# Optimization experiments

Measured on AMD Instinct MI355X. Metric: run time of the kernel, lower is better.

## Reference

```python
import jax, jax.numpy as jnp
import numpy as np

LEAKY_SLOPE = 0.01  # torch nn.LeakyReLU default

def leaky_relu(x):
    return jnp.where(x >= 0, x, LEAKY_SLOPE * x)

def setup_inputs() -> dict:
    key = jax.random.key(0)
    ks = jax.random.split(key, 11)
    B, F, C_IN, H, K, D = 2048, 512, 3, 64, 8, 128  # batch, features, expand, layer_conf[0], bucket_num, bucket_dim
    ASR, MM, OUT = 128, 768, 256
    proj_in = ASR + MM + F * D
    inp = {
        "stat_features": jax.random.uniform(ks[0], (B, F), dtype=jnp.float32),
        "asr_embeddings": jax.random.normal(ks[1], (B, ASR), dtype=jnp.float32),
        "mm_embeddings": jax.random.normal(ks[2], (B, MM), dtype=jnp.float32),
        "linear1_w": jax.random.normal(ks[3], (F, C_IN, H), dtype=jnp.float32) * (1.0 / np.sqrt(C_IN)),
        "linear1_b": jax.random.normal(ks[4], (F, 1, H), dtype=jnp.float32),
        "linear2_w": jax.random.normal(ks[5], (F, H, K), dtype=jnp.float32) * (1.0 / np.sqrt(H)),
        "linear2_b": jax.random.normal(ks[6], (F, 1, K), dtype=jnp.float32),
        "tau": jnp.ones((F, 1, K), dtype=jnp.float32),
        "emb": jax.random.normal(ks[7], (F, K, D), dtype=jnp.float32),
        "proj_w": jax.random.normal(ks[8], (OUT, proj_in), dtype=jnp.float32) * (1.0 / np.sqrt(proj_in)),
        "proj_b": jax.random.normal(ks[9], (OUT,), dtype=jnp.float32) * 0.01,
    }
    return inp

def reference(stat_features, asr_embeddings, mm_embeddings,
              linear1_w, linear1_b, linear2_w, linear2_b, tau, emb,
              proj_w, proj_b):
    # sanitize: NaN -> 0, negatives -> 0
    x = stat_features
    x = jnp.where(jnp.isnan(x) | (x < 0.0), 0.0, x)  # [B, F]

    # auto_dis: per-feature tiny MLP. x is expanded to 3 identical copies -> [B,F,1,3]
    # matmul with [F,3,H] == einsum over the 3 copies.
    B, F = x.shape
    x3 = jnp.broadcast_to(x[:, :, None], (B, F, 3))           # [B,F,3]
    h = jnp.einsum('bfc,fch->bfh', x3, linear1_w) + linear1_b[:, 0, :]  # [B,F,H]
    h = jnp.where(h >= 0, h, LEAKY_SLOPE * h)
    s = jnp.einsum('bfh,fhk->bfk', h, linear2_w) + linear2_b[:, 0, :]   # [B,F,K]
    s = jnp.where(s >= 0, s, LEAKY_SLOPE * s)
    s = s * tau[:, 0, :]
    p = jax.nn.softmax(s, axis=-1)                            # [B,F,K]
    y = jnp.einsum('bfk,fkd->bfd', p, emb)                    # [B,F,D]
    y = y.reshape(B, -1)                                      # [B, F*D] (fc = Identity)

    z = jnp.concatenate([asr_embeddings, mm_embeddings, y], axis=1)
    out = jax.nn.relu(z @ proj_w.T + proj_b)                  # [B, 256]
    return out
```

## Files before the change

kernel.cpp:

```cpp
#include <hip/hip_runtime.h>
#include <hip/hip_bf16.h>
#include <math.h>

#define LEAKY 0.01f
#define B_    2048
#define F_    512
#define H_    64
#define K_    8
#define D_    128
#define ASR_  128
#define MM_   768
#define OUT_  256
#define PROJ_IN 66432
#define ZK    4992
#define NSPLIT 8


typedef unsigned short u16;
typedef u16   u16x8 __attribute__((ext_vector_type(8)));
typedef short s16x8 __attribute__((ext_vector_type(8)));
typedef float f32x4 __attribute__((ext_vector_type(4)));

__device__ __forceinline__ u16 f2bf(float x) {
  unsigned int u = __float_as_uint(x);
  u += 0x7fffu + ((u >> 16) & 1u);
  return (u16)(u >> 16);
}

__device__ __forceinline__ float quad_sum(float g) {
  int a = __builtin_amdgcn_update_dpp(0, __float_as_int(g), 0xB1, 0xF, 0xF, true);
  g += __int_as_float(a);
  int b = __builtin_amdgcn_update_dpp(0, __float_as_int(g), 0x4E, 0xF, 0xF, true);
  return g + __int_as_float(b);
}

#define PRODUCER_BLOCKS (512 + 1024 + 896 + 224)

__global__ __launch_bounds__(256) void producer_kernel(
    const float* __restrict__ stat, const float* __restrict__ w1,
    const float* __restrict__ b1v, const float* __restrict__ w2,
    const float* __restrict__ b2v, const float* __restrict__ tauv,
    const float* __restrict__ pw, const float* __restrict__ emb,
    const float* __restrict__ asr, const float* __restrict__ mm,
    u16* __restrict__ A0, u16* __restrict__ Pf, u16* __restrict__ Wn) {
  __shared__ __align__(16) char smem[15616];
  const int bid = blockIdx.x;
  const int t = threadIdx.x;

  if (bid < 512) {
    const int f0 = (bid >> 3) * 8;
    const int o0 = (bid & 7) * 32;
    const int w = t >> 6, lam = t & 63;
    const int fl = lam >> 5, k = (lam >> 2) & 7, dq = lam & 3;
    const int fbase = f0 + 2 * w;
    float* sw = (float*)smem + w * 512;
    float* buf0 = sw;
    float* buf1 = sw + 256;
    const int wslot = lam ^ ((lam >> 3) & 7);
    const int xr = fl * 4 + dq;
    float4 e[8];
    {
      const float* ep = emb + ((size_t)(fbase + fl) * 8 + k) * 128 + dq * 32;
      #pragma unroll
      for (int j = 0; j < 8; ++j) e[j] = *(const float4*)(ep + j * 4);
    }
    const float* gsrc = pw + 896 + (size_t)fbase * 128
                        + (size_t)o0 * PROJ_IN + lam * 4;
    u16* wdst = Wn + (size_t)o0 * ZK + 896 + (size_t)(fbase + fl) * 8 + k;
    const float* rd0 = buf0 + fl * 128 + dq * 32;
    const float* rd1 = buf1 + fl * 128 + dq * 32;
#define LDR(R) (*(const float4*)(gsrc + (size_t)(R) * PROJ_IN))
#define WNG_ROW(BUF, RD, VREG, R, NEXT)                                       \
    {                                                                         \
      *(float4*)((BUF) + wslot * 4) = VREG;           \
      if ((NEXT) < 32) VREG = LDR(NEXT);                    \
      float g0 = 0.f, g1 = 0.f;                                               \
      _Pragma("unroll")                                                       \
      for (int j = 0; j < 8; ++j) {                                           \
        float4 p4 = *(const float4*)((RD) + 4 * (j ^ xr));                    \
        g0 = fmaf(e[j].x, p4.x, g0);                                          \
        g1 = fmaf(e[j].y, p4.y, g1);                                          \
        g0 = fmaf(e[j].z, p4.z, g0);                                          \
        g1 = fmaf(e[j].w, p4.w, g1);                                          \
      }                                                                       \
      float g = quad_sum(g0 + g1);                                            \
      if (dq == 0) wdst[(size_t)(R) * ZK] = f2bf(g);                          \
    }
    float4 va = LDR(0), vb = LDR(1), vc = LDR(2), vd = LDR(3);
    for (int gi = 0; gi < 8; ++gi) {
      const int r = 4 * gi;
      WNG_ROW(buf0, rd0, va, r,     r + 4);
      WNG_ROW(buf1, rd1, vb, r + 1, r + 5);
      WNG_ROW(buf0, rd0, vc, r + 2, r + 6);
      WNG_ROW(buf1, rd1, vd, r + 3, r + 7);
    }
#undef WNG_ROW
#undef LDR
  } else if (bid < 1536) {
    const int pb = bid - 512;
    const int f0 = (pb & 127) * 4;
    const int b0 = (pb >> 7) * 256;
    float* s_w1s = (float*)(smem);
    float* s_b1  = (float*)(smem + 1024);
    float* s_x   = (float*)(smem + 2048);
    {
      int fl = t >> 6, h = t & 63;
      const float* wf = w1 + (size_t)(f0 + fl) * 192;
      s_w1s[fl * 64 + h] = wf[h] + wf[64 + h] + wf[128 + h];
      s_b1[fl * 64 + h] = b1v[(size_t)(f0 + fl) * 64 + h];
    }
    {
      float4 sv = *(const float4*)(stat + (size_t)(b0 + t) * F_ + f0);
      float* xr_ = s_x + t * 5;
      xr_[0] = (sv.x >= 0.f) ? sv.x : 0.f;
      xr_[1] = (sv.y >= 0.f) ? sv.y : 0.f;
      xr_[2] = (sv.z >= 0.f) ? sv.z : 0.f;
      xr_[3] = (sv.w >= 0.f) ? sv.w : 0.f;
    }
    __syncthreads();

    const int w = t >> 6;
    const int wu = __builtin_amdgcn_readfirstlane(w);
    const int lane = t & 63;
    const float* w1p = s_w1s + w * 64;
    const float* b1p = s_b1 + w * 64;
    const float* w2u  = w2   + (size_t)(f0 + wu) * 512;
    const float* b2u  = b2v  + (size_t)(f0 + wu) * 8;
    const float* tauu = tauv + (size_t)(f0 + wu) * 8;
    float x[4];
    #pragma unroll
    for (int p = 0; p < 4; ++p) x[p] = s_x[(lane + 64 * p) * 5 + w];
    float acc[4][8] = {{0.f}};
    #pragma unroll 4
    for (int i = 0; i < 64; ++i) {
      float wv = w1p[i], bv = b1p[i];
      float4 wa = *(const float4*)(w2u + i * 8);
      float4 wb = *(const float4*)(w2u + i * 8 + 4);
      #pragma unroll
      for (int p = 0; p < 4; ++p) {
        float h0 = fmaf(x[p], wv, bv);
        float h = fmaf(LEAKY, fminf(h0, 0.f), fmaxf(h0, 0.f));
        acc[p][0] = fmaf(h, wa.x, acc[p][0]);
        acc[p][1] = fmaf(h, wa.y, acc[p][1]);
        acc[p][2] = fmaf(h, wa.z, acc[p][2]);
        acc[p][3] = fmaf(h, wa.w, acc[p][3]);
        acc[p][4] = fmaf(h, wb.x, acc[p][4]);
        acc[p][5] = fmaf(h, wb.y, acc[p][5]);
        acc[p][6] = fmaf(h, wb.z, acc[p][6]);
        acc[p][7] = fmaf(h, wb.w, acc[p][7]);
      }
    }
    #pragma unroll
    for (int p = 0; p < 4; ++p) {
      float s[K_];
      float m = -1e30f;
      #pragma unroll
      for (int kk = 0; kk < K_; ++kk) {
        float v = acc[p][kk] + b2u[kk];
        v = (v >= 0.f) ? v : LEAKY * v;
        v *= tauu[kk];
        s[kk] = v;
        m = fmaxf(m, v);
      }
      float sum = 0.f;
      #pragma unroll
      for (int kk = 0; kk < K_; ++kk) { s[kk] = __expf(s[kk] - m); sum += s[kk]; }
      float inv = 1.f / sum;
      u16x8 hv;
      #pragma unroll
      for (int kk = 0; kk < K_; ++kk) hv[kk] = f2bf(s[kk] * inv);
      *(u16x8*)(Pf + ((size_t)(f0 + w) * B_ + b0 + lane + 64 * p) * 8) = hv;
    }
  } else if (bid < 2432) {
    const int item = bid - 1536;
    const int cidx = item * 256 + t;
    const int r = cidx / 112, c = cidx % 112;
    float4 v0, v1;
    if (c < 16) {
      const float* s = asr + (size_t)r * ASR_ + c * 8;
      v0 = *(const float4*)(s); v1 = *(const float4*)(s + 4);
    } else {
      const float* s = mm + (size_t)r * MM_ + (c - 16) * 8;
      v0 = *(const float4*)(s); v1 = *(const float4*)(s + 4);
    }
    u16x8 hv = {f2bf(v0.x), f2bf(v0.y), f2bf(v0.z), f2bf(v0.w),
                f2bf(v1.x), f2bf(v1.y), f2bf(v1.z), f2bf(v1.w)};
    *(u16x8*)(A0 + (size_t)r * 896 + c * 8) = hv;
  } else {
    const int item = bid - 2432;
    #pragma unroll
    for (int rr = 0; rr < 4; ++rr) {
      int idx = item * 1024 + rr * 256 + t;
      int o = idx / 896, j = idx % 896;
      Wn[(size_t)o * ZK + j] = f2bf(pw[(size_t)o * PROJ_IN + j]);
    }
  }
}

#define SAS 72
__global__ __launch_bounds__(256) void gemm_kernel(
    const u16* __restrict__ A0, const u16* __restrict__ Pf,
    const u16* __restrict__ Wn, float* __restrict__ part) {
  const int bm0 = blockIdx.x * 64;
  const int bn0 = blockIdx.y * 64;
  const int kz  = blockIdx.z;
  const int it0 = kz * 10;
  const int itn = (kz == 7) ? 8 : 10;
  __shared__ u16 sA[64 * SAS];
  __shared__ u16 sB[64 * SAS];
  const int t = threadIdx.x;
  const int w = t >> 6, L = t & 63;
  const int l16 = L & 15, q8 = (L >> 4) * 8;
  const int wm = (w >> 1) * 32, wn = (w & 1) * 32;
  const int row = t >> 2, lk = t & 3;
  const int pp = t >> 5, pg = t & 31;
  f32x4 acc[2][2] = {{{0.f,0.f,0.f,0.f},{0.f,0.f,0.f,0.f}},
                     {{0.f,0.f,0.f,0.f},{0.f,0.f,0.f,0.f}}};
  u16x8 ra[2], rb[2];

#define LOAD_TILES(IT)                                                        \
  {                                                                           \
    const int k0_ = (IT) * 64;                                                \
    if (k0_ < 896) {                                                          \
      const u16* s_ = A0 + (size_t)(bm0 + row) * 896 + k0_ + lk * 8;          \
      ra[0] = *(const u16x8*)(s_);                                            \
      ra[1] = *(const u16x8*)(s_ + 32);                                       \
    } else {                                                                  \
      const int fb_ = (k0_ - 896) >> 3;                                       \
      const u16* s_ = Pf + ((size_t)(fb_ + pp) * B_ + bm0 + pg) * 8;          \
      ra[0] = *(const u16x8*)(s_);                                            \
      ra[1] = *(const u16x8*)(s_ + 256);                        \
    }                                                                         \
    const u16* sb_ = Wn + (size_t)(bn0 + row) * ZK + k0_ + lk * 8;            \
    rb[0] = *(const u16x8*)(sb_);                                             \
    rb[1] = *(const u16x8*)(sb_ + 32);                                        \
  }

#define STORE_TILES(IT)                                                       \
  {                                                                           \
    if ((IT) * 64 < 896) {                                                    \
      *(u16x8*)&sA[row * SAS + lk * 8]      = ra[0];                          \
      *(u16x8*)&sA[row * SAS + lk * 8 + 32] = ra[1];                          \
    } else {                                                                  \
      *(u16x8*)&sA[pg * SAS + pp * 8]        = ra[0];                         \
      *(u16x8*)&sA[(pg + 32) * SAS + pp * 8] = ra[1];                         \
    }                                                                         \
    *(u16x8*)&sB[row * SAS + lk * 8]      = rb[0];                            \
    *(u16x8*)&sB[row * SAS + lk * 8 + 32] = rb[1];                            \
  }

  LOAD_TILES(it0);
  for (int it = it0; it < it0 + itn; ++it) {
    __syncthreads();
    STORE_TILES(it);
    __syncthreads();
    if (it + 1 < it0 + itn) LOAD_TILES(it + 1);
    #pragma unroll
    for (int ks = 0; ks < 2; ++ks) {
      s16x8 a0 = *(const s16x8*)&sA[(wm + l16) * SAS + ks * 32 + q8];
      s16x8 a1 = *(const s16x8*)&sA[(wm + 16 + l16) * SAS + ks * 32 + q8];
      s16x8 b0 = *(const s16x8*)&sB[(wn + l16) * SAS + ks * 32 + q8];
      s16x8 b1 = *(const s16x8*)&sB[(wn + 16 + l16) * SAS + ks * 32 + q8];
      acc[0][0] = __builtin_amdgcn_mfma_f32_16x16x32_bf16(a0, b0, acc[0][0], 0, 0, 0);
      acc[0][1] = __builtin_amdgcn_mfma_f32_16x16x32_bf16(a0, b1, acc[0][1], 0, 0, 0);
      acc[1][0] = __builtin_amdgcn_mfma_f32_16x16x32_bf16(a1, b0, acc[1][0], 0, 0, 0);
      acc[1][1] = __builtin_amdgcn_mfma_f32_16x16x32_bf16(a1, b1, acc[1][1], 0, 0, 0);
    }
  }
#undef LOAD_TILES
#undef STORE_TILES

  float* dst = part + (size_t)kz * B_ * OUT_;
  #pragma unroll
  for (int mf = 0; mf < 2; ++mf) {
    const int r0 = bm0 + wm + mf * 16 + (L >> 4) * 4;
    #pragma unroll
    for (int nf = 0; nf < 2; ++nf) {
      const int col = bn0 + wn + nf * 16 + l16;
      #pragma unroll
      for (int i = 0; i < 4; ++i)
        dst[(size_t)(r0 + i) * OUT_ + col] = acc[mf][nf][i];
    }
  }
}

__global__ __launch_bounds__(256) void combine_kernel(
    const float* __restrict__ part, const float* __restrict__ pb,
    float* __restrict__ out) {
  const int idx4 = (blockIdx.x * 256 + threadIdx.x) * 4;
  const int o = idx4 & (OUT_ - 1);
  float4 bv = *(const float4*)(pb + o);
  float4 r = bv;
  #pragma unroll
  for (int kz = 0; kz < NSPLIT; ++kz) {
    float4 a = *(const float4*)(part + (size_t)kz * B_ * OUT_ + idx4);
    r.x += a.x; r.y += a.y; r.z += a.z; r.w += a.w;
  }
  r.x = r.x > 0.f ? r.x : 0.f;
  r.y = r.y > 0.f ? r.y : 0.f;
  r.z = r.z > 0.f ? r.z : 0.f;
  r.w = r.w > 0.f ? r.w : 0.f;
  *(float4*)(out + idx4) = r;
}

extern "C" void kernel_launch(void* const* d_in, const int* in_sizes, int n_in,
                              void* d_out, int out_size, void* d_ws, size_t ws_size,
                              hipStream_t stream) {
  (void)in_sizes; (void)n_in; (void)out_size; (void)ws_size;
  const float* stat = (const float*)d_in[0];
  const float* asr  = (const float*)d_in[1];
  const float* mm   = (const float*)d_in[2];
  const float* w1   = (const float*)d_in[3];
  const float* b1   = (const float*)d_in[4];
  const float* w2   = (const float*)d_in[5];
  const float* b2   = (const float*)d_in[6];
  const float* tau  = (const float*)d_in[7];
  const float* emb  = (const float*)d_in[8];
  const float* pw   = (const float*)d_in[9];
  const float* pb   = (const float*)d_in[10];
  float* out = (float*)d_out;
  char* ws = (char*)d_ws;
  u16*   A0   = (u16*)(ws);
  u16*   Pf   = (u16*)(ws + 3670016);
  u16*   Wn   = (u16*)(ws + 20447232);
  float* part = (float*)(ws + 23003136);

  producer_kernel<<<PRODUCER_BLOCKS, 256, 0, stream>>>(
      stat, w1, b1, w2, b2, tau, pw, emb, asr, mm, A0, Pf, Wn);
  gemm_kernel<<<dim3(B_ / 64, OUT_ / 64, NSPLIT), 256, 0, stream>>>(
      A0, Pf, Wn, part);
  combine_kernel<<<B_ * OUT_ / 1024, 256, 0, stream>>>(part, pb, out);
}
```

Measured before the change: 154.8 us.

## Enlarge GEMM block tile to 128x64 with 32x64 warp tiles

Doubles the M dimension of the split-K GEMM block tile to 128 rows and gives each wave a 32x64 output tile, so every B fragment read from shared memory feeds two MFMAs and each loaded W tile is reused across more rows. The global-to-shared load mapping is rewritten so each thread moves four A vectors and two B vectors per stage. This halves the number of blocks (512 instead of 1024) and raises register and LDS use per block, which can reduce occupancy. The GEMM is small next to the producer kernel, so the effect on total time may be limited.

```diff
diff --git a/kernel.cpp b/kernel.cpp
--- a/kernel.cpp
+++ b/kernel.cpp
@@ -201,52 +201,63 @@
 __global__ __launch_bounds__(256) void gemm_kernel(
     const u16* __restrict__ A0, const u16* __restrict__ Pf,
     const u16* __restrict__ Wn, float* __restrict__ part) {
-  const int bm0 = blockIdx.x * 64;
+  const int bm0 = blockIdx.x * 128;
   const int bn0 = blockIdx.y * 64;
   const int kz  = blockIdx.z;
   const int it0 = kz * 10;
   const int itn = (kz == 7) ? 8 : 10;
-  __shared__ u16 sA[64 * SAS];
+  __shared__ u16 sA[128 * SAS];
   __shared__ u16 sB[64 * SAS];
   const int t = threadIdx.x;
   const int w = t >> 6, L = t & 63;
   const int l16 = L & 15, q8 = (L >> 4) * 8;
-  const int wm = (w >> 1) * 32, wn = (w & 1) * 32;
-  const int row = t >> 2, lk = t & 3;
+  const int wm = w * 32;
+  const int arow = t >> 1, ahalf = t & 1;
   const int pp = t >> 5, pg = t & 31;
-  f32x4 acc[2][2] = {{{0.f,0.f,0.f,0.f},{0.f,0.f,0.f,0.f}},
-                     {{0.f,0.f,0.f,0.f},{0.f,0.f,0.f,0.f}}};
-  u16x8 ra[2], rb[2];
+  const int brow = t >> 2, blk = t & 3;
+  f32x4 acc[2][4] = {{{0.f,0.f,0.f,0.f},{0.f,0.f,0.f,0.f},
+                      {0.f,0.f,0.f,0.f},{0.f,0.f,0.f,0.f}},
+                     {{0.f,0.f,0.f,0.f},{0.f,0.f,0.f,0.f},
+                      {0.f,0.f,0.f,0.f},{0.f,0.f,0.f,0.f}}};
+  u16x8 ra[4], rb[2];
 
 #define LOAD_TILES(IT)                                                        \
   {                                                                           \
     const int k0_ = (IT) * 64;                                                \
     if (k0_ < 896) {                                                          \
-      const u16* s_ = A0 + (size_t)(bm0 + row) * 896 + k0_ + lk * 8;          \
+      const u16* s_ = A0 + (size_t)(bm0 + arow) * 896 + k0_ + ahalf * 32;     \
       ra[0] = *(const u16x8*)(s_);                                            \
-      ra[1] = *(const u16x8*)(s_ + 32);                                       \
+      ra[1] = *(const u16x8*)(s_ + 8);                                        \
+      ra[2] = *(const u16x8*)(s_ + 16);                                       \
+      ra[3] = *(const u16x8*)(s_ + 24);                                       \
     } else {                                                                  \
       const int fb_ = (k0_ - 896) >> 3;                                       \
-      const u16* s_ = Pf + ((size_t)(fb_ + pp) * B_ + bm0 + pg) * 8;          \
+      const u16* s_ = Pf + ((size_t)(fb_ + pp) * B_ + bm0 + pg * 4) * 8;      \
       ra[0] = *(const u16x8*)(s_);                                            \
-      ra[1] = *(const u16x8*)(s_ + 256);                        \
+      ra[1] = *(const u16x8*)(s_ + 8);                                        \
+      ra[2] = *(const u16x8*)(s_ + 16);                                       \
+      ra[3] = *(const u16x8*)(s_ + 24);                                       \
     }                                                                         \
-    const u16* sb_ = Wn + (size_t)(bn0 + row) * ZK + k0_ + lk * 8;            \
+    const u16* sb_ = Wn + (size_t)(bn0 + brow) * ZK + k0_ + blk * 16;         \
     rb[0] = *(const u16x8*)(sb_);                                             \
-    rb[1] = *(const u16x8*)(sb_ + 32);                                        \
+    rb[1] = *(const u16x8*)(sb_ + 8);                                         \
   }
 
 #define STORE_TILES(IT)                                                       \
   {                                                                           \
     if ((IT) * 64 < 896) {                                                    \
-      *(u16x8*)&sA[row * SAS + lk * 8]      = ra[0];                          \
-      *(u16x8*)&sA[row * SAS + lk * 8 + 32] = ra[1];                          \
+      *(u16x8*)&sA[arow * SAS + ahalf * 32]      = ra[0];                     \
+      *(u16x8*)&sA[arow * SAS + ahalf * 32 + 8]  = ra[1];                     \
+      *(u16x8*)&sA[arow * SAS + ahalf * 32 + 16] = ra[2];                     \
+      *(u16x8*)&sA[arow * SAS + ahalf * 32 + 24] = ra[3];                     \
     } else {                                                                  \
-      *(u16x8*)&sA[pg * SAS + pp * 8]        = ra[0];                         \
-      *(u16x8*)&sA[(pg + 32) * SAS + pp * 8] = ra[1];                         \
+      *(u16x8*)&sA[(pg * 4 + 0) * SAS + pp * 8] = ra[0];                      \
+      *(u16x8*)&sA[(pg * 4 + 1) * SAS + pp * 8] = ra[1];                      \
+      *(u16x8*)&sA[(pg * 4 + 2) * SAS + pp * 8] = ra[2];                      \
+      *(u16x8*)&sA[(pg * 4 + 3) * SAS + pp * 8] = ra[3];                      \
     }                                                                         \
-    *(u16x8*)&sB[row * SAS + lk * 8]      = rb[0];                            \
-    *(u16x8*)&sB[row * SAS + lk * 8 + 32] = rb[1];                            \
+    *(u16x8*)&sB[brow * SAS + blk * 16]     = rb[0];                          \
+    *(u16x8*)&sB[brow * SAS + blk * 16 + 8] = rb[1];                          \
   }
 
   LOAD_TILES(it0);
@@ -259,12 +270,12 @@
     for (int ks = 0; ks < 2; ++ks) {
       s16x8 a0 = *(const s16x8*)&sA[(wm + l16) * SAS + ks * 32 + q8];
       s16x8 a1 = *(const s16x8*)&sA[(wm + 16 + l16) * SAS + ks * 32 + q8];
-      s16x8 b0 = *(const s16x8*)&sB[(wn + l16) * SAS + ks * 32 + q8];
-      s16x8 b1 = *(const s16x8*)&sB[(wn + 16 + l16) * SAS + ks * 32 + q8];
-      acc[0][0] = __builtin_amdgcn_mfma_f32_16x16x32_bf16(a0, b0, acc[0][0], 0, 0, 0);
-      acc[0][1] = __builtin_amdgcn_mfma_f32_16x16x32_bf16(a0, b1, acc[0][1], 0, 0, 0);
-      acc[1][0] = __builtin_amdgcn_mfma_f32_16x16x32_bf16(a1, b0, acc[1][0], 0, 0, 0);
-      acc[1][1] = __builtin_amdgcn_mfma_f32_16x16x32_bf16(a1, b1, acc[1][1], 0, 0, 0);
+      #pragma unroll
+      for (int nf = 0; nf < 4; ++nf) {
+        s16x8 b = *(const s16x8*)&sB[(nf * 16 + l16) * SAS + ks * 32 + q8];
+        acc[0][nf] = __builtin_amdgcn_mfma_f32_16x16x32_bf16(a0, b, acc[0][nf], 0, 0, 0);
+        acc[1][nf] = __builtin_amdgcn_mfma_f32_16x16x32_bf16(a1, b, acc[1][nf], 0, 0, 0);
+      }
     }
   }
 #undef LOAD_TILES
@@ -275,8 +286,8 @@
   for (int mf = 0; mf < 2; ++mf) {
     const int r0 = bm0 + wm + mf * 16 + (L >> 4) * 4;
     #pragma unroll
-    for (int nf = 0; nf < 2; ++nf) {
-      const int col = bn0 + wn + nf * 16 + l16;
+    for (int nf = 0; nf < 4; ++nf) {
+      const int col = bn0 + nf * 16 + l16;
       #pragma unroll
       for (int i = 0; i < 4; ++i)
         dst[(size_t)(r0 + i) * OUT_ + col] = acc[mf][nf][i];
@@ -327,7 +338,7 @@
 
   producer_kernel<<<PRODUCER_BLOCKS, 256, 0, stream>>>(
       stat, w1, b1, w2, b2, tau, pw, emb, asr, mm, A0, Pf, Wn);
-  gemm_kernel<<<dim3(B_ / 64, OUT_ / 64, NSPLIT), 256, 0, stream>>>(
+  gemm_kernel<<<dim3(B_ / 128, OUT_ / 64, NSPLIT), 256, 0, stream>>>(
       A0, Pf, Wn, part);
   combine_kernel<<<B_ * OUT_ / 1024, 256, 0, stream>>>(part, pb, out);
 }
```

Result: no change. 154.9 us (+0.0%).
